# Kernel optimization log

Measured on AMD Instinct MI355X. Metric: run time of the kernel, lower is better.

The kernel has to match this reference:

```python
import jax, jax.numpy as jnp
import numpy as np

N = 2_000_000
D = 128
B = 16

def setup_inputs() -> dict:
    key = jax.random.key(0)
    k1, k2 = jax.random.split(key)
    x = jax.random.normal(k1, (N, D), dtype=jnp.float32)
    batch = jnp.sort(jax.random.randint(k2, (N,), 0, B, dtype=jnp.int64))
    return {"x": x, "batch": batch, "num_segments": B}

def reference(x, batch, num_segments):
    # global_mean_pool: segment-mean of x over batch ids.
    sums = jax.ops.segment_sum(x, batch, num_segments=num_segments)  # [B, D]
    counts = jax.ops.segment_sum(jnp.ones((x.shape[0],), dtype=x.dtype), batch,
                                 num_segments=num_segments)          # [B]
    return sums / jnp.maximum(counts, 1.0)[:, None]
```

## Files before the change

### kernel.cpp

```cpp
#include <hip/hip_runtime.h>


#define D       128
#define D4      32
#define BSEG    16
#define BD      (BSEG * D)

#define MB_BLOCKS   512
#define MB_THREADS  512
#define GSTRIDE     (MB_BLOCKS * MB_THREADS)

__global__ __launch_bounds__(256)
void boundary_kernel(const int* __restrict__ batch, int N, int* __restrict__ start)
{
    int stride = gridDim.x * 256;
    for (int i = blockIdx.x * 256 + threadIdx.x; i < N; i += stride) {
        int b = batch[i]; b = min(max(b, 0), BSEG - 1);
        if (i == 0)
            for (int s = 0; s <= b; ++s) start[s] = 0;
        if (i + 1 < N) {
            int c = batch[i + 1]; c = min(max(c, 0), BSEG - 1);
            for (int s = b + 1; s <= c; ++s) start[s] = i + 1;
        } else {
            for (int s = b + 1; s <= BSEG; ++s) start[s] = N;
        }
    }
}

__global__ __launch_bounds__(MB_THREADS)
void pool_main(const float4* __restrict__ x4, const int* __restrict__ start,
               float* __restrict__ partial )
{
    __shared__ float lds_sum[BSEG][D];
    const int tid = threadIdx.x;
    for (int i = tid; i < BD; i += MB_THREADS) ((float*)lds_sum)[i] = 0.0f;
    __syncthreads();

    const int gtid = blockIdx.x * MB_THREADS + tid;
    const int col4 = tid & (D4 - 1);
    const int lane = tid & 63;

    int st[BSEG + 1];
    #pragma unroll
    for (int s = 0; s <= BSEG; ++s) st[s] = start[s];

    #pragma unroll 1
    for (int s = 0; s < BSEG; ++s) {
        const int e1 = st[s + 1] * D4;
        float4 a = make_float4(0.f, 0.f, 0.f, 0.f);
        for (int i = st[s] * D4 + gtid; i < e1; i += GSTRIDE) {
            float4 v = x4[i];
            a.x += v.x; a.y += v.y; a.z += v.z; a.w += v.w;
        }
        a.x += __shfl_down(a.x, 32);
        a.y += __shfl_down(a.y, 32);
        a.z += __shfl_down(a.z, 32);
        a.w += __shfl_down(a.w, 32);
        if (lane < 32) {
            atomicAdd(&lds_sum[s][col4 * 4 + 0], a.x);
            atomicAdd(&lds_sum[s][col4 * 4 + 1], a.y);
            atomicAdd(&lds_sum[s][col4 * 4 + 2], a.z);
            atomicAdd(&lds_sum[s][col4 * 4 + 3], a.w);
        }
    }
    __syncthreads();

    float4* pp = (float4*)(partial + (long)blockIdx.x * BD);
    pp[tid] = ((const float4*)lds_sum)[tid];
}

__global__ __launch_bounds__(256)
void stage2_kernel(const float* __restrict__ partial, float* __restrict__ sums)
{
    int g   = blockIdx.x * 256 + threadIdx.x;
    int col = g & (BD - 1);
    int grp = g >> 11;
    const int rows = MB_BLOCKS / 16;
    int r0 = grp * rows;
    float s = 0.f;
    for (int k = 0; k < rows; ++k)
        s += partial[(r0 + k) * BD + col];
    atomicAdd(&sums[col], s);
}

__global__ __launch_bounds__(256)
void div_kernel(const float* __restrict__ sums, const int* __restrict__ start,
                float* __restrict__ out)
{
    int i = blockIdx.x * 256 + threadIdx.x;
    if (i < BD) {
        int s = i >> 7;
        float c = (float)(start[s + 1] - start[s]);
        out[i] = sums[i] / fmaxf(c, 1.0f);
    }
}

__global__ __launch_bounds__(256)
void pool_sum_fb(const float* __restrict__ x, const int* __restrict__ batch,
                 float* __restrict__ sums, float* __restrict__ counts,
                 int N, int nblocks)
{
    __shared__ float lds_sum[BSEG][D];
    __shared__ float lds_cnt[BSEG];
    const int tid = threadIdx.x;
    for (int i = tid; i < BD; i += 256) ((float*)lds_sum)[i] = 0.0f;
    if (tid < BSEG) lds_cnt[tid] = 0.0f;
    __syncthreads();

    const int chunk = (N + nblocks - 1) / nblocks;
    const int r0 = blockIdx.x * chunk;
    int r1 = r0 + chunk; if (r1 > N) r1 = N;
    const int col4 = tid & (D4 - 1);
    const int rlane = tid >> 5;
    const float4* x4 = (const float4*)x;

    float4 acc = make_float4(0.f, 0.f, 0.f, 0.f);
    int cnt = 0, cur = -1;
    for (int r = r0 + rlane; r < r1; r += 8) {
        int seg = batch[r];
        if (seg != cur) {
            if (cur >= 0) {
                atomicAdd(&lds_sum[cur][col4 * 4 + 0], acc.x);
                atomicAdd(&lds_sum[cur][col4 * 4 + 1], acc.y);
                atomicAdd(&lds_sum[cur][col4 * 4 + 2], acc.z);
                atomicAdd(&lds_sum[cur][col4 * 4 + 3], acc.w);
                if (col4 == 0) atomicAdd(&lds_cnt[cur], (float)cnt);
            }
            acc = make_float4(0.f, 0.f, 0.f, 0.f); cnt = 0;
            cur = (seg >= 0 && seg < BSEG) ? seg : -1;
        }
        if (cur >= 0) {
            float4 v = x4[(long)r * D4 + col4];
            acc.x += v.x; acc.y += v.y; acc.z += v.z; acc.w += v.w; cnt++;
        }
    }
    if (cur >= 0) {
        atomicAdd(&lds_sum[cur][col4 * 4 + 0], acc.x);
        atomicAdd(&lds_sum[cur][col4 * 4 + 1], acc.y);
        atomicAdd(&lds_sum[cur][col4 * 4 + 2], acc.z);
        atomicAdd(&lds_sum[cur][col4 * 4 + 3], acc.w);
        if (col4 == 0) atomicAdd(&lds_cnt[cur], (float)cnt);
    }
    __syncthreads();
    for (int i = tid; i < BD; i += 256) {
        float v = ((float*)lds_sum)[i];
        if (v != 0.0f) atomicAdd(&sums[i], v);
    }
    if (tid < BSEG) {
        float c = lds_cnt[tid];
        if (c != 0.0f) atomicAdd(&counts[tid], c);
    }
}

__global__ __launch_bounds__(256)
void div_fb(const float* __restrict__ sums, const float* __restrict__ counts,
            float* __restrict__ out)
{
    int i = blockIdx.x * 256 + threadIdx.x;
    if (i < BD) out[i] = sums[i] / fmaxf(counts[i >> 7], 1.0f);
}

extern "C" void kernel_launch(void* const* d_in, const int* in_sizes, int n_in,
                              void* d_out, int out_size, void* d_ws, size_t ws_size,
                              hipStream_t stream)
{
    const float* x     = (const float*)d_in[0];
    const int*   batch = (const int*)d_in[1];
    const int    N     = in_sizes[1];

    int*   start   = (int*)d_ws;
    float* sums    = (float*)d_ws + 32;
    float* partial = (float*)d_ws + 32 + BD;
    const size_t need = (size_t)(32 + BD + (size_t)MB_BLOCKS * BD) * sizeof(float);

    if (ws_size >= need) {
        hipMemsetAsync(sums, 0, BD * sizeof(float), stream);
        boundary_kernel<<<2048, 256, 0, stream>>>(batch, N, start);
        pool_main<<<MB_BLOCKS, MB_THREADS, 0, stream>>>((const float4*)x, start, partial);
        stage2_kernel<<<128, 256, 0, stream>>>(partial, sums);
        div_kernel<<<8, 256, 0, stream>>>(sums, start, (float*)d_out);
    } else {
        float* fsums   = (float*)d_ws;
        float* fcounts = fsums + BD;
        hipMemsetAsync(d_ws, 0, (BD + BSEG) * sizeof(float), stream);
        pool_sum_fb<<<2048, 256, 0, stream>>>(x, batch, fsums, fcounts, N, 2048);
        div_fb<<<8, 256, 0, stream>>>(fsums, fcounts, (float*)d_out);
    }
}
```

Before: 200.9 us.

## Double main-kernel block size, vectorize boundary scan, stage segment starts in LDS

The main pooling kernel now runs 1024 threads per block, doubling the grid-stride parallelism over x, with a launch-bounds occupancy hint. Segment start offsets are loaded once into shared memory instead of per-thread registers. The boundary kernel now reads four batch ids per thread with an int4 load and launches one thread per four rows instead of a grid-stride loop. This aims to raise memory-level parallelism on the 1 GB streaming read and cut boundary-scan overhead. The int4 load assumes batch is 16-byte aligned, and the final partial write is guarded because the block is now larger than the partial tile.

```diff
diff --git a/kernel.cpp b/kernel.cpp
--- a/kernel.cpp
+++ b/kernel.cpp
@@ -7,48 +7,61 @@
 #define BD      (BSEG * D)
 
 #define MB_BLOCKS   512
-#define MB_THREADS  512
+#define MB_THREADS  1024
 #define GSTRIDE     (MB_BLOCKS * MB_THREADS)
 
 __global__ __launch_bounds__(256)
 void boundary_kernel(const int* __restrict__ batch, int N, int* __restrict__ start)
 {
-    int stride = gridDim.x * 256;
-    for (int i = blockIdx.x * 256 + threadIdx.x; i < N; i += stride) {
-        int b = batch[i]; b = min(max(b, 0), BSEG - 1);
-        if (i == 0)
-            for (int s = 0; s <= b; ++s) start[s] = 0;
-        if (i + 1 < N) {
-            int c = batch[i + 1]; c = min(max(c, 0), BSEG - 1);
-            for (int s = b + 1; s <= c; ++s) start[s] = i + 1;
-        } else {
-            for (int s = b + 1; s <= BSEG; ++s) start[s] = N;
-        }
-    }
-}
-
-__global__ __launch_bounds__(MB_THREADS)
+    int t  = blockIdx.x * 256 + threadIdx.x;
+    int i0 = t * 4;
+    if (i0 >= N) return;
+
+    int e[5];
+    if (i0 + 4 <= N) {
+        int4 b = *(const int4*)(batch + i0);
+        e[0] = b.x; e[1] = b.y; e[2] = b.z; e[3] = b.w;
+    } else {
+        for (int k = 0; k < 4; ++k) e[k] = (i0 + k < N) ? batch[i0 + k] : batch[N - 1];
+    }
+    bool last = (i0 + 4 >= N);
+    e[4] = last ? BSEG : batch[i0 + 4];
+
+    if (i0 == 0) {
+        int b0 = min(max(e[0], 0), BSEG - 1);
+        for (int s = 0; s <= b0; ++s) start[s] = 0;
+    }
+    for (int k = 0; k < 4; ++k) {
+        int a = min(max(e[k], 0), BSEG - 1);
+        int b = (k == 3) ? (last ? BSEG : min(max(e[4], 0), BSEG - 1))
+                         : min(max(e[k + 1], 0), BSEG - 1);
+        int pos = i0 + k + 1; if (pos > N) pos = N;
+        for (int s = a + 1; s <= b; ++s) start[s] = pos;
+    }
+}
+
+__global__ __launch_bounds__(MB_THREADS, 8)
 void pool_main(const float4* __restrict__ x4, const int* __restrict__ start,
                float* __restrict__ partial )
 {
     __shared__ float lds_sum[BSEG][D];
+    __shared__ int   lds_st[BSEG + 1];
+
     const int tid = threadIdx.x;
     for (int i = tid; i < BD; i += MB_THREADS) ((float*)lds_sum)[i] = 0.0f;
+    if (tid <= BSEG) lds_st[tid] = start[tid];
     __syncthreads();
 
     const int gtid = blockIdx.x * MB_THREADS + tid;
     const int col4 = tid & (D4 - 1);
     const int lane = tid & 63;
 
-    int st[BSEG + 1];
-    #pragma unroll
-    for (int s = 0; s <= BSEG; ++s) st[s] = start[s];
-
     #pragma unroll 1
     for (int s = 0; s < BSEG; ++s) {
-        const int e1 = st[s + 1] * D4;
+        const int i0 = lds_st[s] * D4 + gtid;
+        const int e1 = lds_st[s + 1] * D4;
         float4 a = make_float4(0.f, 0.f, 0.f, 0.f);
-        for (int i = st[s] * D4 + gtid; i < e1; i += GSTRIDE) {
+        for (int i = i0; i < e1; i += GSTRIDE) {
             float4 v = x4[i];
             a.x += v.x; a.y += v.y; a.z += v.z; a.w += v.w;
         }
@@ -65,8 +78,10 @@
     }
     __syncthreads();
 
-    float4* pp = (float4*)(partial + (long)blockIdx.x * BD);
-    pp[tid] = ((const float4*)lds_sum)[tid];
+    if (tid < BD / 4) {
+        float4* pp = (float4*)(partial + (long)blockIdx.x * BD);
+        pp[tid] = ((const float4*)lds_sum)[tid];
+    }
 }
 
 __global__ __launch_bounds__(256)
@@ -175,7 +190,7 @@
 
     if (ws_size >= need) {
         hipMemsetAsync(sums, 0, BD * sizeof(float), stream);
-        boundary_kernel<<<2048, 256, 0, stream>>>(batch, N, start);
+        boundary_kernel<<<(N / 4 + 255) / 256, 256, 0, stream>>>(batch, N, start);
         pool_main<<<MB_BLOCKS, MB_THREADS, 0, stream>>>((const float4*)x, start, partial);
         stage2_kernel<<<128, 256, 0, stream>>>(partial, sums);
         div_kernel<<<8, 256, 0, stream>>>(sums, start, (float*)d_out);
```

Result: faster. 193.9 us (-3.5%).
